# Optimization experiments

Hardware: AMD Instinct MI355X
Metric: run time of the kernel (lower is better)

Reference implementation:

```python
import jax, jax.numpy as jnp
import numpy as np

N_NODES = 50000
N_EDGES = 600000
IN_CH = 64
HID = 128
N_GRAPHS = 64
EPS = 0.0  # GINEConv default eps


def setup_inputs() -> dict:
    key = jax.random.key(0)
    ks = jax.random.split(key, 16)
    x = jax.random.normal(ks[0], (N_NODES, IN_CH), dtype=jnp.float32)
    edge_index = jax.random.randint(ks[1], (2, N_EDGES), 0, N_NODES, dtype=jnp.int64)
    edge_attr = jax.random.normal(ks[2], (N_EDGES, 3), dtype=jnp.float32)
    batch = jnp.sort(jax.random.randint(ks[3], (N_NODES,), 0, N_GRAPHS, dtype=jnp.int64))
    s = lambda fan_in: 1.0 / np.sqrt(fan_in)
    # conv1: edge lin (3->IN_CH), mlp (IN_CH->HID->HID)
    el1_w = jax.random.uniform(ks[4], (3, IN_CH), minval=-s(3), maxval=s(3))
    el1_b = jnp.zeros((IN_CH,), jnp.float32)
    w1a = jax.random.uniform(ks[5], (IN_CH, HID), minval=-s(IN_CH), maxval=s(IN_CH))
    b1a = jnp.zeros((HID,), jnp.float32)
    w1b = jax.random.uniform(ks[6], (HID, HID), minval=-s(HID), maxval=s(HID))
    b1b = jnp.zeros((HID,), jnp.float32)
    # conv2: edge lin (3->HID), mlp (HID->HID->HID)
    el2_w = jax.random.uniform(ks[7], (3, HID), minval=-s(3), maxval=s(3))
    el2_b = jnp.zeros((HID,), jnp.float32)
    w2a = jax.random.uniform(ks[8], (HID, HID), minval=-s(HID), maxval=s(HID))
    b2a = jnp.zeros((HID,), jnp.float32)
    w2b = jax.random.uniform(ks[9], (HID, HID), minval=-s(HID), maxval=s(HID))
    b2b = jnp.zeros((HID,), jnp.float32)
    return dict(x=x, edge_index=edge_index, edge_attr=edge_attr, batch=batch,
                el1_w=el1_w, el1_b=el1_b, w1a=w1a, b1a=b1a, w1b=w1b, b1b=b1b,
                el2_w=el2_w, el2_b=el2_b, w2a=w2a, b2a=b2a, w2b=w2b, b2b=b2b)


def _gine_conv(x, src, dst, edge_attr, el_w, el_b, wa, ba, wb, bb):
    # message: relu(x_j + Lin(edge_attr)), aggregated (sum) at target nodes
    e = edge_attr @ el_w + el_b              # [E, d]
    msg = jax.nn.relu(x[src] + e)            # [E, d]
    agg = jax.ops.segment_sum(msg, dst, num_segments=x.shape[0])  # [N, d]
    h = (1.0 + EPS) * x + agg
    h = jax.nn.relu(h @ wa + ba) @ wb + bb   # MLP
    return h


def reference(x, edge_index, edge_attr, batch,
              el1_w, el1_b, w1a, b1a, w1b, b1b,
              el2_w, el2_b, w2a, b2a, w2b, b2b):
    src, dst = edge_index[0], edge_index[1]
    h = jax.nn.relu(_gine_conv(x, src, dst, edge_attr, el1_w, el1_b, w1a, b1a, w1b, b1b))
    h = jax.nn.relu(_gine_conv(h, src, dst, edge_attr, el2_w, el2_b, w2a, b2a, w2b, b2b))
    # global mean pool per graph
    sums = jax.ops.segment_sum(h, batch, num_segments=N_GRAPHS)
    cnt = jax.ops.segment_sum(jnp.ones((h.shape[0],), h.dtype), batch, num_segments=N_GRAPHS)
    return sums / jnp.maximum(cnt, 1.0)[:, None]
```

## Files before the change

### kernel.cpp

```cpp
#include <hip/hip_runtime.h>

#define N_NODES 50000
#define N_EDGES 600000
#define N_PAD 50048
#define IN_CH 64
#define HID 128
#define N_GRAPHS 64
#define SCAN_BLOCKS 196

typedef __attribute__((ext_vector_type(8))) short bf16x8;
typedef __attribute__((ext_vector_type(4))) float f32x4;

__device__ __forceinline__ float bf2f(unsigned short u) {
    union { unsigned int i; float f; } v; v.i = ((unsigned int)u) << 16; return v.f;
}
__device__ __forceinline__ unsigned short f2bf(float f) {
    union { float f; unsigned int i; } v; v.f = f;
    unsigned int u = v.i;
    return (unsigned short)((u + 0x7FFFu + ((u >> 16) & 1u)) >> 16);
}
__device__ __forceinline__ float rowval(float f) { return f; }
__device__ __forceinline__ float rowval(unsigned short u) { return bf2f(u); }

template <bool B> struct RowType { using T = float; };
template <> struct RowType<true> { using T = unsigned short; };

__global__ void hist_kernel(const int* __restrict__ ei, int* __restrict__ deg) {
    int e = blockIdx.x * blockDim.x + threadIdx.x;
    if (e < N_EDGES) atomicAdd(&deg[ei[N_EDGES + e]], 1);
}

__device__ __forceinline__ int block_incl_scan256(int v, int* sm, int t) {
    int val = v;
    sm[t] = val; __syncthreads();
    #pragma unroll
    for (int off = 1; off < 256; off <<= 1) {
        int n = (t >= off) ? sm[t - off] : 0;
        __syncthreads();
        val += n; sm[t] = val; __syncthreads();
    }
    return val;
}

__global__ void scan1_kernel(const int* __restrict__ deg, int* __restrict__ partials) {
    __shared__ int sm[256];
    int t = threadIdx.x;
    int i = blockIdx.x * 256 + t;
    int v = (i < N_NODES) ? deg[i] : 0;
    sm[t] = v; __syncthreads();
    for (int off = 128; off > 0; off >>= 1) {
        if (t < off) sm[t] += sm[t + off];
        __syncthreads();
    }
    if (t == 0) partials[blockIdx.x] = sm[0];
}

__global__ void scan2_kernel(int* __restrict__ partials) {
    __shared__ int sm[256];
    int t = threadIdx.x;
    int v = (t < SCAN_BLOCKS) ? partials[t] : 0;
    int incl = block_incl_scan256(v, sm, t);
    if (t < SCAN_BLOCKS) partials[t] = incl - v;
}

__global__ void scan3_kernel(const int* __restrict__ deg,
                             const int* __restrict__ partials,
                             int* __restrict__ rowptr,
                             int* __restrict__ cursor) {
    __shared__ int sm[256];
    int t = threadIdx.x;
    int i = blockIdx.x * 256 + t;
    int v = (i < N_NODES) ? deg[i] : 0;
    int incl = block_incl_scan256(v, sm, t);
    int excl = incl - v + partials[blockIdx.x];
    if (i < N_NODES) { rowptr[i] = excl; cursor[i] = excl; }
    if (blockIdx.x == 0 && t == 0) rowptr[N_NODES] = N_EDGES;
}

__global__ void scatter_kernel(const int* __restrict__ ei,
                               const float* __restrict__ ea,
                               int* __restrict__ cursor,
                               int4* __restrict__ edata) {
    int e = blockIdx.x * blockDim.x + threadIdx.x;
    if (e < N_EDGES) {
        int dst = ei[N_EDGES + e];
        int pos = atomicAdd(&cursor[dst], 1);
        edata[pos] = make_int4(ei[e],
                               __float_as_int(ea[3 * e]),
                               __float_as_int(ea[3 * e + 1]),
                               __float_as_int(ea[3 * e + 2]));
    }
}

__global__ void tw_kernel(const float* __restrict__ w, unsigned short* __restrict__ wT,
                          int Kdim, int Ndim) {
    int i = blockIdx.x * blockDim.x + threadIdx.x;
    if (i < Kdim * Ndim) {
        int k = i / Ndim, n = i % Ndim;
        wT[n * Kdim + k] = f2bf(w[k * Ndim + n]);
    }
}

template <int K, bool XBF>
__global__ void gather_kernel(const void* __restrict__ xinv,
                              const int4* __restrict__ edata,
                              const int* __restrict__ rowptr,
                              const float* __restrict__ elw,
                              const float* __restrict__ elb,
                              unsigned short* __restrict__ sg) {
    using RowT = typename RowType<XBF>::T;
    const RowT* __restrict__ xin = (const RowT*)xinv;
    constexpr int NPB = 8;
    const int node0 = blockIdx.x * NPB;
    const int t = threadIdx.x;

    const int c = (K == 128) ? t : (t & 63);
    const int half = (K == 128) ? 0 : (t >> 6);
    const int istep = (K == 128) ? 1 : 2;
    const float w0 = elw[c], w1 = elw[K + c], w2 = elw[2 * K + c], eb = elb[c];

    auto term = [&](int4 e, RowT row) -> float {
        float ev = __int_as_float(e.y) * w0 + __int_as_float(e.z) * w1 +
                   __int_as_float(e.w) * w2 + eb;
        float m = rowval(row) + ev;
        return m > 0.f ? m : 0.f;
    };

    for (int i = 0; i < NPB; i += istep) {
        int node = node0 + i + half;
        float acc = rowval(xin[(size_t)node * K + c]);
        int jb = rowptr[node], je = rowptr[node + 1];
        int j = jb;
        for (; j + 8 <= je; j += 8) {
            int4 e0 = edata[j],     e1 = edata[j + 1], e2 = edata[j + 2], e3 = edata[j + 3];
            int4 e4 = edata[j + 4], e5 = edata[j + 5], e6 = edata[j + 6], e7 = edata[j + 7];
            RowT r0 = xin[(size_t)e0.x * K + c];
            RowT r1 = xin[(size_t)e1.x * K + c];
            RowT r2 = xin[(size_t)e2.x * K + c];
            RowT r3 = xin[(size_t)e3.x * K + c];
            RowT r4 = xin[(size_t)e4.x * K + c];
            RowT r5 = xin[(size_t)e5.x * K + c];
            RowT r6 = xin[(size_t)e6.x * K + c];
            RowT r7 = xin[(size_t)e7.x * K + c];
            acc += term(e0, r0) + term(e1, r1) + term(e2, r2) + term(e3, r3)
                 + term(e4, r4) + term(e5, r5) + term(e6, r6) + term(e7, r7);
        }
        for (; j + 4 <= je; j += 4) {
            int4 e0 = edata[j], e1 = edata[j + 1], e2 = edata[j + 2], e3 = edata[j + 3];
            RowT r0 = xin[(size_t)e0.x * K + c];
            RowT r1 = xin[(size_t)e1.x * K + c];
            RowT r2 = xin[(size_t)e2.x * K + c];
            RowT r3 = xin[(size_t)e3.x * K + c];
            acc += term(e0, r0) + term(e1, r1) + term(e2, r2) + term(e3, r3);
        }
        for (; j < je; j++) {
            int4 e0 = edata[j];
            acc += term(e0, xin[(size_t)e0.x * K + c]);
        }
        sg[(size_t)node * K + c] = f2bf(acc);
    }
}

template <int K, bool POOL>
__global__ __launch_bounds__(256)
void mlp_mfma_kernel(const unsigned short* __restrict__ sg,
                     const unsigned short* __restrict__ waT,
                     const float* __restrict__ ba,
                     const unsigned short* __restrict__ wbT,
                     const float* __restrict__ bb,
                     void* __restrict__ outv,
                     const int* __restrict__ batch) {
    constexpr int HSTR = 136;
    constexpr int OSTR = HID + 4;
    __shared__ __align__(16) unsigned short sHid[4][16 * HSTR];
    __shared__ __align__(16) float sOut[64 * OSTR];
    const int t = threadIdx.x;
    const int w = t >> 6, l = t & 63;
    const int i16 = l & 15, q = l >> 4;
    const int blk0 = blockIdx.x * 64;
    const int row0 = blk0 + w * 16;

    bf16x8 aA[K / 32];
    #pragma unroll
    for (int s = 0; s < K / 32; s++)
        aA[s] = *(const bf16x8*)&sg[(size_t)(row0 + i16) * K + s * 32 + q * 8];
    unsigned short* myHid = sHid[w];
    #pragma unroll
    for (int ct = 0; ct < 8; ct++) {
        int col = ct * 16 + i16;
        float bv = ba[col];
        f32x4 acc = (f32x4){bv, bv, bv, bv};
        #pragma unroll
        for (int s = 0; s < K / 32; s++) {
            bf16x8 b = *(const bf16x8*)&waT[(size_t)col * K + s * 32 + q * 8];
            acc = __builtin_amdgcn_mfma_f32_16x16x32_bf16(aA[s], b, acc, 0, 0, 0);
        }
        #pragma unroll
        for (int r = 0; r < 4; r++) {
            float v = acc[r] > 0.f ? acc[r] : 0.f;
            myHid[(q * 4 + r) * HSTR + col] = f2bf(v);
        }
    }
    __syncthreads();

    bf16x8 aB[4];
    #pragma unroll
    for (int s = 0; s < 4; s++)
        aB[s] = *(const bf16x8*)&myHid[i16 * HSTR + s * 32 + q * 8];
    #pragma unroll
    for (int ct = 0; ct < 8; ct++) {
        int col = ct * 16 + i16;
        float bv = bb[col];
        f32x4 acc = (f32x4){bv, bv, bv, bv};
        #pragma unroll
        for (int s = 0; s < 4; s++) {
            bf16x8 b = *(const bf16x8*)&wbT[(size_t)col * HID + s * 32 + q * 8];
            acc = __builtin_amdgcn_mfma_f32_16x16x32_bf16(aB[s], b, acc, 0, 0, 0);
        }
        #pragma unroll
        for (int r = 0; r < 4; r++) {
            float v = acc[r] > 0.f ? acc[r] : 0.f;
            sOut[(w * 16 + q * 4 + r) * OSTR + col] = v;
        }
    }
    __syncthreads();

    if (POOL) {
        if (t < HID) {
            float* psum = (float*)outv;
            float acc = 0.f;
            int curg = batch[blk0];
            for (int row = 0; row < 64; row++) {
                int node = blk0 + row;
                if (node >= N_NODES) break;
                int g = batch[node];
                if (g != curg) {
                    atomicAdd(&psum[curg * HID + t], acc);
                    acc = 0.f; curg = g;
                }
                acc += sOut[row * OSTR + t];
            }
            atomicAdd(&psum[curg * HID + t], acc);
        }
    } else {
        unsigned short* hout = (unsigned short*)outv;
        for (int idx = t; idx < 64 * 16; idx += 256) {
            int row = idx >> 4, ch = idx & 15;
            int node = blk0 + row;
            if (node < N_NODES) {
                float4 f0 = *(const float4*)&sOut[row * OSTR + ch * 8];
                float4 f1 = *(const float4*)&sOut[row * OSTR + ch * 8 + 4];
                uint4 u;
                u.x = (unsigned)f2bf(f0.x) | ((unsigned)f2bf(f0.y) << 16);
                u.y = (unsigned)f2bf(f0.z) | ((unsigned)f2bf(f0.w) << 16);
                u.z = (unsigned)f2bf(f1.x) | ((unsigned)f2bf(f1.y) << 16);
                u.w = (unsigned)f2bf(f1.z) | ((unsigned)f2bf(f1.w) << 16);
                *(uint4*)&hout[(size_t)node * HID + ch * 8] = u;
            }
        }
    }
}

__global__ void pool_div_kernel(const float* __restrict__ sums,
                                const int* __restrict__ batch,
                                float* __restrict__ out) {
    int i = blockIdx.x * blockDim.x + threadIdx.x;
    if (i >= N_GRAPHS * HID) return;
    int g = i / HID;
    int lo = 0, hi = N_NODES;
    while (lo < hi) { int mid = (lo + hi) >> 1; if (batch[mid] < g) lo = mid + 1; else hi = mid; }
    int start = lo;
    lo = 0; hi = N_NODES;
    while (lo < hi) { int mid = (lo + hi) >> 1; if (batch[mid] <= g) lo = mid + 1; else hi = mid; }
    float c = (float)(lo - start);
    out[i] = sums[i] / (c > 1.0f ? c : 1.0f);
}

extern "C" void kernel_launch(void* const* d_in, const int* in_sizes, int n_in,
                              void* d_out, int out_size, void* d_ws, size_t ws_size,
                              hipStream_t stream) {
    const float* x    = (const float*)d_in[0];
    const int*   ei   = (const int*)d_in[1];
    const float* ea   = (const float*)d_in[2];
    const int*   batch= (const int*)d_in[3];
    const float* el1w = (const float*)d_in[4];
    const float* el1b = (const float*)d_in[5];
    const float* w1a  = (const float*)d_in[6];
    const float* b1a  = (const float*)d_in[7];
    const float* w1b  = (const float*)d_in[8];
    const float* b1b  = (const float*)d_in[9];
    const float* el2w = (const float*)d_in[10];
    const float* el2b = (const float*)d_in[11];
    const float* w2a  = (const float*)d_in[12];
    const float* b2a  = (const float*)d_in[13];
    const float* w2b  = (const float*)d_in[14];
    const float* b2b  = (const float*)d_in[15];
    float* out = (float*)d_out;

    int4*  edata    = (int4*)d_ws;
    float* psum     = (float*)(edata + N_EDGES);
    int*   deg      = (int*)(psum + N_GRAPHS * HID);
    int*   cursor   = deg + N_NODES;
    int*   rowptr   = cursor + N_NODES;
    int*   partials = rowptr + N_NODES + 1;
    unsigned short* hbf  = (unsigned short*)((char*)psum + (size_t)158452 * 4);
    unsigned short* sgbuf= hbf + (size_t)N_NODES * HID;
    unsigned short* waT1 = sgbuf + (size_t)N_PAD * HID;
    unsigned short* wbT1 = waT1 + HID * IN_CH;
    unsigned short* waT2 = wbT1 + HID * HID;
    unsigned short* wbT2 = waT2 + HID * HID;

    hipMemsetAsync(deg, 0, N_NODES * sizeof(int), stream);
    hist_kernel<<<(N_EDGES + 255) / 256, 256, 0, stream>>>(ei, deg);
    tw_kernel<<<(IN_CH * HID + 255) / 256, 256, 0, stream>>>(w1a, waT1, IN_CH, HID);
    tw_kernel<<<(HID * HID + 255) / 256, 256, 0, stream>>>(w1b, wbT1, HID, HID);
    tw_kernel<<<(HID * HID + 255) / 256, 256, 0, stream>>>(w2a, waT2, HID, HID);
    tw_kernel<<<(HID * HID + 255) / 256, 256, 0, stream>>>(w2b, wbT2, HID, HID);
    scan1_kernel<<<SCAN_BLOCKS, 256, 0, stream>>>(deg, partials);
    scan2_kernel<<<1, 256, 0, stream>>>(partials);
    scan3_kernel<<<SCAN_BLOCKS, 256, 0, stream>>>(deg, partials, rowptr, cursor);
    scatter_kernel<<<(N_EDGES + 255) / 256, 256, 0, stream>>>(ei, ea, cursor, edata);

    gather_kernel<IN_CH, false><<<N_NODES / 8, 128, 0, stream>>>(
        x, edata, rowptr, el1w, el1b, sgbuf);
    mlp_mfma_kernel<IN_CH, false><<<N_PAD / 64, 256, 0, stream>>>(
        sgbuf, waT1, b1a, wbT1, b1b, hbf, nullptr);

    hipMemsetAsync(psum, 0, N_GRAPHS * HID * sizeof(float), stream);
    gather_kernel<HID, true><<<N_NODES / 8, 128, 0, stream>>>(
        hbf, edata, rowptr, el2w, el2b, sgbuf);
    mlp_mfma_kernel<HID, true><<<N_PAD / 64, 256, 0, stream>>>(
        sgbuf, waT2, b2a, wbT2, b2b, psum, batch);

    pool_div_kernel<<<(N_GRAPHS * HID + 255) / 256, 256, 0, stream>>>(psum, batch, out);
}
```

Before: 321.0 us.

## Gather layer-2 bf16 rows with one wave per node and merge prep launches

The layer-2 gather now assigns a whole 64-lane wave to each node. Each lane loads a packed pair of bf16 channels as one 32-bit word, where before each thread read a single 16-bit channel. This halves the number of load instructions per gathered row and gives each wave its own node instead of one node per 128-thread block. The two memsets and four weight-transpose launches are also merged into one prep kernel to cut launch overhead. The trade-off is more register work per lane and a different block/node mapping (16 nodes per 256-thread block).

```diff
diff --git a/kernel.cpp b/kernel.cpp
--- a/kernel.cpp
+++ b/kernel.cpp
@@ -19,11 +19,26 @@
     unsigned int u = v.i;
     return (unsigned short)((u + 0x7FFFu + ((u >> 16) & 1u)) >> 16);
 }
-__device__ __forceinline__ float rowval(float f) { return f; }
-__device__ __forceinline__ float rowval(unsigned short u) { return bf2f(u); }
-
-template <bool B> struct RowType { using T = float; };
-template <> struct RowType<true> { using T = unsigned short; };
+
+__global__ void prep_kernel(const float* __restrict__ w1a, const float* __restrict__ w1b,
+                            const float* __restrict__ w2a, const float* __restrict__ w2b,
+                            unsigned short* __restrict__ waT1, unsigned short* __restrict__ wbT1,
+                            unsigned short* __restrict__ waT2, unsigned short* __restrict__ wbT2,
+                            int* __restrict__ deg, float* __restrict__ psum) {
+    int i = blockIdx.x * blockDim.x + threadIdx.x;
+    if (i < N_NODES) deg[i] = 0;
+    if (i < N_GRAPHS * HID) psum[i] = 0.f;
+    if (i < IN_CH * HID) {
+        int k = i / HID, n = i % HID;
+        waT1[n * IN_CH + k] = f2bf(w1a[i]);
+    }
+    if (i < HID * HID) {
+        int k = i / HID, n = i % HID;
+        wbT1[n * HID + k] = f2bf(w1b[i]);
+        waT2[n * HID + k] = f2bf(w2a[i]);
+        wbT2[n * HID + k] = f2bf(w2b[i]);
+    }
+}
 
 __global__ void hist_kernel(const int* __restrict__ ei, int* __restrict__ deg) {
     int e = blockIdx.x * blockDim.x + threadIdx.x;
@@ -92,65 +107,51 @@
     }
 }
 
-__global__ void tw_kernel(const float* __restrict__ w, unsigned short* __restrict__ wT,
-                          int Kdim, int Ndim) {
-    int i = blockIdx.x * blockDim.x + threadIdx.x;
-    if (i < Kdim * Ndim) {
-        int k = i / Ndim, n = i % Ndim;
-        wT[n * Kdim + k] = f2bf(w[k * Ndim + n]);
-    }
-}
-
-template <int K, bool XBF>
-__global__ void gather_kernel(const void* __restrict__ xinv,
-                              const int4* __restrict__ edata,
-                              const int* __restrict__ rowptr,
-                              const float* __restrict__ elw,
-                              const float* __restrict__ elb,
-                              unsigned short* __restrict__ sg) {
-    using RowT = typename RowType<XBF>::T;
-    const RowT* __restrict__ xin = (const RowT*)xinv;
+__global__ void gather64_kernel(const float* __restrict__ xin,
+                                const int4* __restrict__ edata,
+                                const int* __restrict__ rowptr,
+                                const float* __restrict__ elw,
+                                const float* __restrict__ elb,
+                                unsigned short* __restrict__ sg) {
+    constexpr int K = IN_CH;
     constexpr int NPB = 8;
     const int node0 = blockIdx.x * NPB;
     const int t = threadIdx.x;
-
-    const int c = (K == 128) ? t : (t & 63);
-    const int half = (K == 128) ? 0 : (t >> 6);
-    const int istep = (K == 128) ? 1 : 2;
+    const int c = t & 63, half = t >> 6;
     const float w0 = elw[c], w1 = elw[K + c], w2 = elw[2 * K + c], eb = elb[c];
 
-    auto term = [&](int4 e, RowT row) -> float {
+    auto term = [&](int4 e, float row) -> float {
         float ev = __int_as_float(e.y) * w0 + __int_as_float(e.z) * w1 +
                    __int_as_float(e.w) * w2 + eb;
-        float m = rowval(row) + ev;
+        float m = row + ev;
         return m > 0.f ? m : 0.f;
     };
 
-    for (int i = 0; i < NPB; i += istep) {
+    for (int i = 0; i < NPB; i += 2) {
         int node = node0 + i + half;
-        float acc = rowval(xin[(size_t)node * K + c]);
+        float acc = xin[(size_t)node * K + c];
         int jb = rowptr[node], je = rowptr[node + 1];
         int j = jb;
         for (; j + 8 <= je; j += 8) {
             int4 e0 = edata[j],     e1 = edata[j + 1], e2 = edata[j + 2], e3 = edata[j + 3];
             int4 e4 = edata[j + 4], e5 = edata[j + 5], e6 = edata[j + 6], e7 = edata[j + 7];
-            RowT r0 = xin[(size_t)e0.x * K + c];
-            RowT r1 = xin[(size_t)e1.x * K + c];
-            RowT r2 = xin[(size_t)e2.x * K + c];
-            RowT r3 = xin[(size_t)e3.x * K + c];
-            RowT r4 = xin[(size_t)e4.x * K + c];
-            RowT r5 = xin[(size_t)e5.x * K + c];
-            RowT r6 = xin[(size_t)e6.x * K + c];
-            RowT r7 = xin[(size_t)e7.x * K + c];
+            float r0 = xin[(size_t)e0.x * K + c];
+            float r1 = xin[(size_t)e1.x * K + c];
+            float r2 = xin[(size_t)e2.x * K + c];
+            float r3 = xin[(size_t)e3.x * K + c];
+            float r4 = xin[(size_t)e4.x * K + c];
+            float r5 = xin[(size_t)e5.x * K + c];
+            float r6 = xin[(size_t)e6.x * K + c];
+            float r7 = xin[(size_t)e7.x * K + c];
             acc += term(e0, r0) + term(e1, r1) + term(e2, r2) + term(e3, r3)
                  + term(e4, r4) + term(e5, r5) + term(e6, r6) + term(e7, r7);
         }
         for (; j + 4 <= je; j += 4) {
             int4 e0 = edata[j], e1 = edata[j + 1], e2 = edata[j + 2], e3 = edata[j + 3];
-            RowT r0 = xin[(size_t)e0.x * K + c];
-            RowT r1 = xin[(size_t)e1.x * K + c];
-            RowT r2 = xin[(size_t)e2.x * K + c];
-            RowT r3 = xin[(size_t)e3.x * K + c];
+            float r0 = xin[(size_t)e0.x * K + c];
+            float r1 = xin[(size_t)e1.x * K + c];
+            float r2 = xin[(size_t)e2.x * K + c];
+            float r3 = xin[(size_t)e3.x * K + c];
             acc += term(e0, r0) + term(e1, r1) + term(e2, r2) + term(e3, r3);
         }
         for (; j < je; j++) {
@@ -158,6 +159,70 @@
             acc += term(e0, xin[(size_t)e0.x * K + c]);
         }
         sg[(size_t)node * K + c] = f2bf(acc);
+    }
+}
+
+__global__ void gather128_kernel(const unsigned short* __restrict__ xin,
+                                 const int4* __restrict__ edata,
+                                 const int* __restrict__ rowptr,
+                                 const float* __restrict__ elw,
+                                 const float* __restrict__ elb,
+                                 unsigned short* __restrict__ sg) {
+    constexpr int NPW = 4;
+    const int t = threadIdx.x;
+    const int w = t >> 6, l = t & 63;
+    const unsigned* x32 = (const unsigned*)xin;
+    unsigned* sg32 = (unsigned*)sg;
+    const int c0 = 2 * l;
+    const float w00 = elw[c0],           w01 = elw[c0 + 1];
+    const float w10 = elw[HID + c0],     w11 = elw[HID + c0 + 1];
+    const float w20 = elw[2 * HID + c0], w21 = elw[2 * HID + c0 + 1];
+    const float eb0 = elb[c0],           eb1 = elb[c0 + 1];
+    const int node0 = (blockIdx.x * 4 + w) * NPW;
+
+    for (int ni = 0; ni < NPW; ni++) {
+        int node = node0 + ni;
+        unsigned sv = x32[(size_t)node * 64 + l];
+        float acc0 = bf2f((unsigned short)(sv & 0xFFFF));
+        float acc1 = bf2f((unsigned short)(sv >> 16));
+        auto term2 = [&](int4 e, unsigned r) {
+            float A0 = __int_as_float(e.y), A1 = __int_as_float(e.z), A2 = __int_as_float(e.w);
+            float ev0 = A0 * w00 + A1 * w10 + A2 * w20 + eb0;
+            float ev1 = A0 * w01 + A1 * w11 + A2 * w21 + eb1;
+            float m0 = bf2f((unsigned short)(r & 0xFFFF)) + ev0;
+            float m1 = bf2f((unsigned short)(r >> 16)) + ev1;
+            acc0 += m0 > 0.f ? m0 : 0.f;
+            acc1 += m1 > 0.f ? m1 : 0.f;
+        };
+        int jb = rowptr[node], je = rowptr[node + 1];
+        int j = jb;
+        for (; j + 8 <= je; j += 8) {
+            int4 e0 = edata[j],     e1 = edata[j + 1], e2 = edata[j + 2], e3 = edata[j + 3];
+            int4 e4 = edata[j + 4], e5 = edata[j + 5], e6 = edata[j + 6], e7 = edata[j + 7];
+            unsigned r0 = x32[(size_t)e0.x * 64 + l];
+            unsigned r1 = x32[(size_t)e1.x * 64 + l];
+            unsigned r2 = x32[(size_t)e2.x * 64 + l];
+            unsigned r3 = x32[(size_t)e3.x * 64 + l];
+            unsigned r4 = x32[(size_t)e4.x * 64 + l];
+            unsigned r5 = x32[(size_t)e5.x * 64 + l];
+            unsigned r6 = x32[(size_t)e6.x * 64 + l];
+            unsigned r7 = x32[(size_t)e7.x * 64 + l];
+            term2(e0, r0); term2(e1, r1); term2(e2, r2); term2(e3, r3);
+            term2(e4, r4); term2(e5, r5); term2(e6, r6); term2(e7, r7);
+        }
+        for (; j + 4 <= je; j += 4) {
+            int4 e0 = edata[j], e1 = edata[j + 1], e2 = edata[j + 2], e3 = edata[j + 3];
+            unsigned r0 = x32[(size_t)e0.x * 64 + l];
+            unsigned r1 = x32[(size_t)e1.x * 64 + l];
+            unsigned r2 = x32[(size_t)e2.x * 64 + l];
+            unsigned r3 = x32[(size_t)e3.x * 64 + l];
+            term2(e0, r0); term2(e1, r1); term2(e2, r2); term2(e3, r3);
+        }
+        for (; j < je; j++) {
+            int4 e0 = edata[j];
+            term2(e0, x32[(size_t)e0.x * 64 + l]);
+        }
+        sg32[(size_t)node * 64 + l] = (unsigned)f2bf(acc0) | ((unsigned)f2bf(acc1) << 16);
     }
 }
 
@@ -310,24 +375,20 @@
     unsigned short* waT2 = wbT1 + HID * HID;
     unsigned short* wbT2 = waT2 + HID * HID;
 
-    hipMemsetAsync(deg, 0, N_NODES * sizeof(int), stream);
+    prep_kernel<<<(N_NODES + 255) / 256, 256, 0, stream>>>(
+        w1a, w1b, w2a, w2b, waT1, wbT1, waT2, wbT2, deg, psum);
     hist_kernel<<<(N_EDGES + 255) / 256, 256, 0, stream>>>(ei, deg);
-    tw_kernel<<<(IN_CH * HID + 255) / 256, 256, 0, stream>>>(w1a, waT1, IN_CH, HID);
-    tw_kernel<<<(HID * HID + 255) / 256, 256, 0, stream>>>(w1b, wbT1, HID, HID);
-    tw_kernel<<<(HID * HID + 255) / 256, 256, 0, stream>>>(w2a, waT2, HID, HID);
-    tw_kernel<<<(HID * HID + 255) / 256, 256, 0, stream>>>(w2b, wbT2, HID, HID);
     scan1_kernel<<<SCAN_BLOCKS, 256, 0, stream>>>(deg, partials);
     scan2_kernel<<<1, 256, 0, stream>>>(partials);
     scan3_kernel<<<SCAN_BLOCKS, 256, 0, stream>>>(deg, partials, rowptr, cursor);
     scatter_kernel<<<(N_EDGES + 255) / 256, 256, 0, stream>>>(ei, ea, cursor, edata);
 
-    gather_kernel<IN_CH, false><<<N_NODES / 8, 128, 0, stream>>>(
+    gather64_kernel<<<N_NODES / 8, 128, 0, stream>>>(
         x, edata, rowptr, el1w, el1b, sgbuf);
     mlp_mfma_kernel<IN_CH, false><<<N_PAD / 64, 256, 0, stream>>>(
         sgbuf, waT1, b1a, wbT1, b1b, hbf, nullptr);
 
-    hipMemsetAsync(psum, 0, N_GRAPHS * HID * sizeof(float), stream);
-    gather_kernel<HID, true><<<N_NODES / 8, 128, 0, stream>>>(
+    gather128_kernel<<<N_NODES / 16, 256, 0, stream>>>(
         hbf, edata, rowptr, el2w, el2b, sgbuf);
     mlp_mfma_kernel<HID, true><<<N_PAD / 64, 256, 0, stream>>>(
         sgbuf, waT2, b2a, wbT2, b2b, psum, batch);
```

Result: faster. 308.3 us (-4.0%).
